# Optimization experiments

Measured on AMD Instinct MI355X. Metric: run time of the kernel, lower is better.

## Reference

```python
import jax, jax.numpy as jnp
import numpy as np

N_NODES = 100000
N_FEAT = 256
HIDDEN = 16
N_CLASSES = 16
N_EDGES = 3200000


def setup_inputs() -> dict:
    key = jax.random.key(0)
    k = jax.random.split(key, 7)
    x = jax.random.normal(k[0], (N_NODES, N_FEAT), dtype=jnp.float32)
    edge_index = jax.random.randint(k[1], (2, N_EDGES), 0, N_NODES, dtype=jnp.int32)
    # GCNConv: linear (no bias) + bias added after aggregation
    s1 = 1.0 / np.sqrt(N_FEAT)
    W1 = jax.random.uniform(k[2], (N_FEAT, HIDDEN), jnp.float32, -s1, s1)
    b1 = jnp.zeros((HIDDEN,), jnp.float32)
    # SAGEConv: lin_l (on aggregated neighbors, with bias) + lin_r (root)
    s2 = 1.0 / np.sqrt(HIDDEN)
    Wl = jax.random.uniform(k[3], (HIDDEN, N_CLASSES), jnp.float32, -s2, s2)
    Wr = jax.random.uniform(k[4], (HIDDEN, N_CLASSES), jnp.float32, -s2, s2)
    b2 = jax.random.uniform(k[5], (N_CLASSES,), jnp.float32, -s2, s2)
    return {"x": x, "edge_index": edge_index, "W1": W1, "b1": b1,
            "Wl": Wl, "Wr": Wr, "b2": b2}


def reference(x, edge_index, W1, b1, Wl, Wr, b2):
    N = x.shape[0]
    src, dst = edge_index[0], edge_index[1]

    # ---- GCNConv(num_features -> hidden): transform, add self-loops,
    # symmetric normalization, sum-aggregate, add bias ----
    h = x @ W1  # [N, H]
    loop = jnp.arange(N, dtype=src.dtype)
    src2 = jnp.concatenate([src, loop])
    dst2 = jnp.concatenate([dst, loop])
    ones = jnp.ones(src2.shape[0], dtype=h.dtype)
    deg = jax.ops.segment_sum(ones, dst2, num_segments=N)  # in-degree incl. self-loop
    dinv = jnp.where(deg > 0, jax.lax.rsqrt(deg), 0.0)
    norm = dinv[src2] * dinv[dst2]  # [E+N]
    msgs = h[src2] * norm[:, None]
    h1 = jax.ops.segment_sum(msgs, dst2, num_segments=N) + b1  # [N, H]

    # ---- SAGEConv(hidden -> num_classes, aggr='mean') ----
    cnt = jax.ops.segment_sum(jnp.ones(src.shape[0], dtype=h1.dtype), dst, num_segments=N)
    agg = jax.ops.segment_sum(h1[src], dst, num_segments=N)
    agg = agg / jnp.maximum(cnt, 1.0)[:, None]  # mean over neighbors
    out = agg @ Wl + h1 @ Wr + b2  # [N, C]

    return jax.nn.log_softmax(out, axis=1)
```

## Files before the change

### kernel.cpp

```cpp
#include <hip/hip_runtime.h>
#include <cstddef>

#define NF 256
#define NH 16
#define NC 16

#define BN    128
#define BSH   7
#define BMSK  127
#define CAP   4608
#define AVLEN 32
#define ACH   (256*AVLEN)
#define NBMAX 800

typedef __attribute__((ext_vector_type(8))) short bf16x8;
typedef __attribute__((ext_vector_type(4))) float f32x4;

__device__ inline short f2bf(float f) {
    union { float f; unsigned int u; } v; v.f = f;
    const unsigned int r = v.u + 0x7FFFu + ((v.u >> 16) & 1u);
    return (short)(r >> 16);
}
__device__ inline float bf2f(unsigned short u) {
    union { unsigned int i; float f; } v; v.i = ((unsigned int)u) << 16;
    return v.f;
}

__global__ __launch_bounds__(256) void bucketA_kernel(
    const int* __restrict__ src, const int* __restrict__ dst,
    unsigned int* __restrict__ bfill, unsigned int* __restrict__ bpairs,
    int E, int NBK)
{
    __shared__ unsigned int hist[NBMAX];
    __shared__ unsigned int sbase[NBMAX];
    __shared__ unsigned int gpos[NBMAX];
    __shared__ unsigned int tmp[1024];
    __shared__ unsigned int reorder[ACH];
    __shared__ unsigned short wbid[ACH];

    const int tid = threadIdx.x;
    for (int i = tid; i < NBMAX; i += 256) hist[i] = 0u;
    __syncthreads();

    const int base = blockIdx.x * ACH;
    unsigned int pv[AVLEN];
    unsigned int ps[AVLEN];
    #pragma unroll
    for (int l = 0; l < AVLEN; ++l) {
        const int e = base + l * 256 + tid;
        if (e < E) {
            const unsigned int s = (unsigned int)src[e];
            const unsigned int d = (unsigned int)dst[e];
            const unsigned int b = d >> BSH;
            pv[l] = (s << BSH) | (d & BMSK);
            const unsigned int slot = atomicAdd(&hist[b], 1u);
            ps[l] = (slot << 10) | b;
        } else {
            ps[l] = 0xFFFFFFFFu;
        }
    }
    __syncthreads();

    for (int i = tid; i < 1024; i += 256) tmp[i] = (i < NBK) ? hist[i] : 0u;
    __syncthreads();
    for (int off = 1; off < 1024; off <<= 1) {
        unsigned int v0 = 0, v1 = 0, v2 = 0, v3 = 0;
        const int i0 = tid, i1 = tid + 256, i2 = tid + 512, i3 = tid + 768;
        if (i0 >= off) v0 = tmp[i0 - off];
        if (i1 >= off) v1 = tmp[i1 - off];
        if (i2 >= off) v2 = tmp[i2 - off];
        if (i3 >= off) v3 = tmp[i3 - off];
        __syncthreads();
        tmp[i0] += v0; tmp[i1] += v1; tmp[i2] += v2; tmp[i3] += v3;
        __syncthreads();
    }
    for (int i = tid; i < NBK; i += 256) {
        const unsigned int h = hist[i];
        sbase[i] = tmp[i] - h;
        if (h) gpos[i] = atomicAdd(&bfill[i], h);
    }
    const int cc = (base + ACH <= E) ? ACH : (E - base);
    __syncthreads();

    #pragma unroll
    for (int l = 0; l < AVLEN; ++l) {
        if (ps[l] != 0xFFFFFFFFu) {
            const unsigned int b = ps[l] & 1023u;
            const unsigned int i = sbase[b] + (ps[l] >> 10);
            reorder[i] = pv[l];
            wbid[i] = (unsigned short)b;
        }
    }
    __syncthreads();

    for (int i = tid; i < cc; i += 256) {
        const unsigned int b = wbid[i];
        const unsigned int g = gpos[b] + ((unsigned int)i - sbase[b]);
        if (g < CAP) bpairs[(size_t)b * CAP + g] = reorder[i];
    }
}

__global__ __launch_bounds__(256) void bucketB_kernel(
    const unsigned int* __restrict__ bfill, unsigned int* __restrict__ bpairs,
    int* __restrict__ rowptr, int* __restrict__ cnt, float* __restrict__ dinv,
    int N)
{
    __shared__ unsigned int pairs[CAP];
    __shared__ unsigned int ssorted[CAP];
    __shared__ unsigned int hist[BN];
    __shared__ unsigned int scan[BN];
    __shared__ unsigned int cursor[BN];

    const int tid = threadIdx.x;
    const int b = blockIdx.x;
    const size_t bbase = (size_t)b * CAP;
    unsigned int m = bfill[b]; if (m > CAP) m = CAP;

    if (tid < BN) hist[tid] = 0u;
    __syncthreads();

    for (unsigned int i = tid; i < m; i += 256) {
        const unsigned int p = bpairs[bbase + i];
        pairs[i] = p;
        atomicAdd(&hist[p & BMSK], 1u);
    }
    __syncthreads();

    if (tid < BN) scan[tid] = hist[tid];
    __syncthreads();
    for (int off = 1; off < BN; off <<= 1) {
        unsigned int v = 0;
        if (tid < BN && tid >= off) v = scan[tid - off];
        __syncthreads();
        if (tid < BN) scan[tid] += v;
        __syncthreads();
    }
    if (tid < BN) cursor[tid] = scan[tid] - hist[tid];
    __syncthreads();

    for (unsigned int i = tid; i < m; i += 256) {
        const unsigned int p = pairs[i];
        const unsigned int pos = atomicAdd(&cursor[p & BMSK], 1u);
        ssorted[pos] = p >> BSH;
    }
    __syncthreads();

    for (unsigned int i = tid; i < m; i += 256)
        bpairs[bbase + i] = ssorted[i];

    if (tid < BN) {
        const int n = b * BN + tid;
        if (n < N) {
            const unsigned int h = hist[tid];
            cnt[n] = (int)h;
            dinv[n] = rsqrtf((float)h + 1.0f);
            rowptr[n] = (int)(b * CAP + (scan[tid] - h));
        }
    }
}

__global__ __launch_bounds__(256) void gemm1_mfma_kernel(
    const float* __restrict__ x, const float* __restrict__ W1,
    const float* __restrict__ dinv, unsigned short* __restrict__ hs_bf, int N)
{
    const int lane = threadIdx.x & 63;
    const int wave = threadIdx.x >> 6;
    const int quad = lane >> 4;
    const int mn   = lane & 15;

    bf16x8 bfrag[8];
    #pragma unroll
    for (int kc = 0; kc < 8; ++kc) {
        #pragma unroll
        for (int j = 0; j < 8; ++j) {
            const int k = kc * 32 + quad * 8 + j;
            bfrag[kc][j] = f2bf(W1[k * NH + mn]);
        }
    }

    const int tile = blockIdx.x * 4 + wave;
    if (tile * 16 >= N) return;
    const int n0 = tile * 16;

    f32x4 acc = {0.f, 0.f, 0.f, 0.f};
    const float* xrow = x + (size_t)(n0 + mn) * NF + quad * 8;
    #pragma unroll
    for (int kc = 0; kc < 8; ++kc) {
        const float4 lo = *(const float4*)(xrow + kc * 32);
        const float4 hi = *(const float4*)(xrow + kc * 32 + 4);
        bf16x8 af;
        af[0] = f2bf(lo.x); af[1] = f2bf(lo.y); af[2] = f2bf(lo.z); af[3] = f2bf(lo.w);
        af[4] = f2bf(hi.x); af[5] = f2bf(hi.y); af[6] = f2bf(hi.z); af[7] = f2bf(hi.w);
        acc = __builtin_amdgcn_mfma_f32_16x16x32_bf16(af, bfrag[kc], acc, 0, 0, 0);
    }

    const float4 dv = *(const float4*)(dinv + n0 + quad * 4);
    const float d[4] = {dv.x, dv.y, dv.z, dv.w};
    #pragma unroll
    for (int r = 0; r < 4; ++r) {
        const int row = quad * 4 + r;
        hs_bf[(size_t)(n0 + row) * NH + mn] = (unsigned short)f2bf(acc[r] * d[r]);
    }
}

__global__ __launch_bounds__(256) void gcn_gather_kernel(
    const unsigned short* __restrict__ hs_bf, const unsigned int* __restrict__ csrc,
    const int* __restrict__ rowptr, const int* __restrict__ cnt,
    const float* __restrict__ dinv, const float* __restrict__ b1,
    unsigned short* __restrict__ h1_bf, int N)
{
    const int tid = threadIdx.x;
    const int n = blockIdx.x * 16 + (tid >> 4);
    if (n >= N) return;
    const int j = tid & 15;
    const int start = rowptr[n];
    const int end = start + cnt[n];

    float acc = bf2f(hs_bf[(size_t)n * NH + j]);
    int k = start;
    for (; k + 16 <= end; k += 16) {
        const int myi = (int)csrc[k + j];
        float s = 0.f;
        #pragma unroll
        for (int u = 0; u < 16; ++u) {
            const int sidx = __shfl(myi, u, 16);
            s += bf2f(hs_bf[(size_t)sidx * NH + j]);
        }
        acc += s;
    }
    for (; k < end; ++k)
        acc += bf2f(hs_bf[(size_t)csrc[k] * NH + j]);

    h1_bf[(size_t)n * NH + j] = (unsigned short)f2bf(b1[j] + dinv[n] * acc);
}

__global__ __launch_bounds__(256) void sage_out_kernel(
    const unsigned short* __restrict__ h1_bf, const unsigned int* __restrict__ csrc,
    const int* __restrict__ rowptr, const int* __restrict__ cnt,
    const float* __restrict__ Wl, const float* __restrict__ Wr,
    const float* __restrict__ b2, float* __restrict__ out, int N)
{
    __shared__ float wls[NH * NC];
    __shared__ float wrs[NH * NC];
    __shared__ float b2s[NC];
    const int tid = threadIdx.x;
    if (tid < NH * NC) { wls[tid] = Wl[tid]; wrs[tid] = Wr[tid]; }
    if (tid < NC) b2s[tid] = b2[tid];
    __syncthreads();

    const int n = blockIdx.x * 16 + (tid >> 4);
    if (n >= N) return;
    const int j = tid & 15;
    const int start = rowptr[n];
    const int deg = cnt[n];
    const int end = start + deg;

    float acc = 0.f;
    int k = start;
    for (; k + 16 <= end; k += 16) {
        const int myi = (int)csrc[k + j];
        float s = 0.f;
        #pragma unroll
        for (int u = 0; u < 16; ++u) {
            const int sidx = __shfl(myi, u, 16);
            s += bf2f(h1_bf[(size_t)sidx * NH + j]);
        }
        acc += s;
    }
    for (; k < end; ++k)
        acc += bf2f(h1_bf[(size_t)csrc[k] * NH + j]);

    const float aggj = acc / fmaxf((float)deg, 1.0f);
    const float h1j  = bf2f(h1_bf[(size_t)n * NH + j]);

    float o = b2s[j];
    #pragma unroll
    for (int kk = 0; kk < NH; ++kk) {
        const float a  = __shfl(aggj, kk, 16);
        const float hh = __shfl(h1j,  kk, 16);
        o += a * wls[kk * NC + j] + hh * wrs[kk * NC + j];
    }

    float m = o;
    #pragma unroll
    for (int off = 1; off < 16; off <<= 1) m = fmaxf(m, __shfl_xor(m, off, 16));
    const float ex = expf(o - m);
    float ssum = ex;
    #pragma unroll
    for (int off = 1; off < 16; off <<= 1) ssum += __shfl_xor(ssum, off, 16);

    out[(size_t)n * NC + j] = (o - m) - logf(ssum);
}

extern "C" void kernel_launch(void* const* d_in, const int* in_sizes, int n_in,
                              void* d_out, int out_size, void* d_ws, size_t ws_size,
                              hipStream_t stream)
{
    const float* x  = (const float*)d_in[0];
    const int*   ei = (const int*)d_in[1];
    const float* W1 = (const float*)d_in[2];
    const float* b1 = (const float*)d_in[3];
    const float* Wl = (const float*)d_in[4];
    const float* Wr = (const float*)d_in[5];
    const float* b2 = (const float*)d_in[6];
    float* out = (float*)d_out;

    const int N = in_sizes[0] / NF;
    const int E = in_sizes[1] / 2;
    const int* src = ei;
    const int* dst = ei + E;

    const int NBK = (N + BN - 1) / BN;

    unsigned short* hs_bf = (unsigned short*)d_ws;
    unsigned short* h1_bf = hs_bf + (size_t)N * NH;
    float* dinv   = (float*)(h1_bf + (size_t)N * NH);
    int*   cnt    = (int*)(dinv + N);
    int*   rowptr = cnt + N;
    unsigned int* bfill  = (unsigned int*)(rowptr + N);
    unsigned int* bpairs = bfill + 1024;

    hipMemsetAsync(bfill, 0, (size_t)NBK * sizeof(unsigned int), stream);

    bucketA_kernel<<<(E + ACH - 1) / ACH, 256, 0, stream>>>(src, dst, bfill, bpairs, E, NBK);
    bucketB_kernel<<<NBK, 256, 0, stream>>>(bfill, bpairs, rowptr, cnt, dinv, N);

    const int tiles = (N + 15) / 16;
    gemm1_mfma_kernel<<<(tiles + 3) / 4, 256, 0, stream>>>(x, W1, dinv, hs_bf, N);

    const int nodeBlk = (N + 15) / 16;
    gcn_gather_kernel<<<nodeBlk, 256, 0, stream>>>(hs_bf, bpairs, rowptr, cnt, dinv, b1, h1_bf, N);
    sage_out_kernel<<<nodeBlk, 256, 0, stream>>>(h1_bf, bpairs, rowptr, cnt, Wl, Wr, b2, out, N);
}
```

Measured before the change: 319.2 us.

## Sub-sort edges by source range, use nontemporal accesses, shrink bucketing chunk

Bucket sort now orders each destination's edges into 8 sub-bins by the high bits of the source index, aiming to improve gather locality in the aggregation kernels. Streaming loads and stores of edge lists, x, and output use nontemporal hints to reduce cache pollution. The first bucketing pass halves its per-block chunk, which raises block count and lowers register pressure. The trade-off is a larger 1024-entry scan in the second pass and more partial-bucket writes.

```diff
diff --git a/kernel.cpp b/kernel.cpp
--- a/kernel.cpp
+++ b/kernel.cpp
@@ -9,9 +9,11 @@
 #define BSH   7
 #define BMSK  127
 #define CAP   4608
-#define AVLEN 32
+#define AVLEN 16
 #define ACH   (256*AVLEN)
 #define NBMAX 800
+#define NW    8
+#define SWSH  14
 
 typedef __attribute__((ext_vector_type(8))) short bf16x8;
 typedef __attribute__((ext_vector_type(4))) float f32x4;
@@ -49,8 +51,8 @@
     for (int l = 0; l < AVLEN; ++l) {
         const int e = base + l * 256 + tid;
         if (e < E) {
-            const unsigned int s = (unsigned int)src[e];
-            const unsigned int d = (unsigned int)dst[e];
+            const unsigned int s = (unsigned int)__builtin_nontemporal_load(&src[e]);
+            const unsigned int d = (unsigned int)__builtin_nontemporal_load(&dst[e]);
             const unsigned int b = d >> BSH;
             pv[l] = (s << BSH) | (d & BMSK);
             const unsigned int slot = atomicAdd(&hist[b], 1u);
@@ -107,54 +109,62 @@
 {
     __shared__ unsigned int pairs[CAP];
     __shared__ unsigned int ssorted[CAP];
-    __shared__ unsigned int hist[BN];
-    __shared__ unsigned int scan[BN];
-    __shared__ unsigned int cursor[BN];
+    __shared__ unsigned int hist[BN * NW];
+    __shared__ unsigned int scan[BN * NW];
+    __shared__ unsigned int cursor[BN * NW];
 
     const int tid = threadIdx.x;
     const int b = blockIdx.x;
     const size_t bbase = (size_t)b * CAP;
     unsigned int m = bfill[b]; if (m > CAP) m = CAP;
 
-    if (tid < BN) hist[tid] = 0u;
+    for (int i = tid; i < BN * NW; i += 256) hist[i] = 0u;
     __syncthreads();
 
     for (unsigned int i = tid; i < m; i += 256) {
-        const unsigned int p = bpairs[bbase + i];
+        const unsigned int p = __builtin_nontemporal_load(&bpairs[bbase + i]);
         pairs[i] = p;
-        atomicAdd(&hist[p & BMSK], 1u);
-    }
-    __syncthreads();
-
-    if (tid < BN) scan[tid] = hist[tid];
-    __syncthreads();
-    for (int off = 1; off < BN; off <<= 1) {
-        unsigned int v = 0;
-        if (tid < BN && tid >= off) v = scan[tid - off];
+        const unsigned int key = ((p & BMSK) << 3) | ((p >> BSH) >> SWSH);
+        atomicAdd(&hist[key], 1u);
+    }
+    __syncthreads();
+
+    for (int i = tid; i < 1024; i += 256) scan[i] = hist[i];
+    __syncthreads();
+    for (int off = 1; off < 1024; off <<= 1) {
+        unsigned int v0 = 0, v1 = 0, v2 = 0, v3 = 0;
+        const int i0 = tid, i1 = tid + 256, i2 = tid + 512, i3 = tid + 768;
+        if (i0 >= off) v0 = scan[i0 - off];
+        if (i1 >= off) v1 = scan[i1 - off];
+        if (i2 >= off) v2 = scan[i2 - off];
+        if (i3 >= off) v3 = scan[i3 - off];
         __syncthreads();
-        if (tid < BN) scan[tid] += v;
+        scan[i0] += v0; scan[i1] += v1; scan[i2] += v2; scan[i3] += v3;
         __syncthreads();
     }
-    if (tid < BN) cursor[tid] = scan[tid] - hist[tid];
+    for (int i = tid; i < 1024; i += 256) cursor[i] = scan[i] - hist[i];
     __syncthreads();
 
     for (unsigned int i = tid; i < m; i += 256) {
         const unsigned int p = pairs[i];
-        const unsigned int pos = atomicAdd(&cursor[p & BMSK], 1u);
+        const unsigned int key = ((p & BMSK) << 3) | ((p >> BSH) >> SWSH);
+        const unsigned int pos = atomicAdd(&cursor[key], 1u);
         ssorted[pos] = p >> BSH;
     }
     __syncthreads();
 
     for (unsigned int i = tid; i < m; i += 256)
-        bpairs[bbase + i] = ssorted[i];
+        __builtin_nontemporal_store(ssorted[i], &bpairs[bbase + i]);
 
     if (tid < BN) {
         const int n = b * BN + tid;
         if (n < N) {
-            const unsigned int h = hist[tid];
+            unsigned int h = 0;
+            #pragma unroll
+            for (int w = 0; w < NW; ++w) h += hist[tid * NW + w];
             cnt[n] = (int)h;
             dinv[n] = rsqrtf((float)h + 1.0f);
-            rowptr[n] = (int)(b * CAP + (scan[tid] - h));
+            rowptr[n] = (int)(b * CAP + (scan[tid * NW] - hist[tid * NW]));
         }
     }
 }
@@ -186,20 +196,19 @@
     const float* xrow = x + (size_t)(n0 + mn) * NF + quad * 8;
     #pragma unroll
     for (int kc = 0; kc < 8; ++kc) {
-        const float4 lo = *(const float4*)(xrow + kc * 32);
-        const float4 hi = *(const float4*)(xrow + kc * 32 + 4);
+        const f32x4 lo = __builtin_nontemporal_load((const f32x4*)(xrow + kc * 32));
+        const f32x4 hi = __builtin_nontemporal_load((const f32x4*)(xrow + kc * 32 + 4));
         bf16x8 af;
-        af[0] = f2bf(lo.x); af[1] = f2bf(lo.y); af[2] = f2bf(lo.z); af[3] = f2bf(lo.w);
-        af[4] = f2bf(hi.x); af[5] = f2bf(hi.y); af[6] = f2bf(hi.z); af[7] = f2bf(hi.w);
+        af[0] = f2bf(lo[0]); af[1] = f2bf(lo[1]); af[2] = f2bf(lo[2]); af[3] = f2bf(lo[3]);
+        af[4] = f2bf(hi[0]); af[5] = f2bf(hi[1]); af[6] = f2bf(hi[2]); af[7] = f2bf(hi[3]);
         acc = __builtin_amdgcn_mfma_f32_16x16x32_bf16(af, bfrag[kc], acc, 0, 0, 0);
     }
 
-    const float4 dv = *(const float4*)(dinv + n0 + quad * 4);
-    const float d[4] = {dv.x, dv.y, dv.z, dv.w};
+    const f32x4 dv = *(const f32x4*)(dinv + n0 + quad * 4);
     #pragma unroll
     for (int r = 0; r < 4; ++r) {
         const int row = quad * 4 + r;
-        hs_bf[(size_t)(n0 + row) * NH + mn] = (unsigned short)f2bf(acc[r] * d[r]);
+        hs_bf[(size_t)(n0 + row) * NH + mn] = (unsigned short)f2bf(acc[r] * dv[r]);
     }
 }
 
@@ -219,7 +228,7 @@
     float acc = bf2f(hs_bf[(size_t)n * NH + j]);
     int k = start;
     for (; k + 16 <= end; k += 16) {
-        const int myi = (int)csrc[k + j];
+        const int myi = (int)__builtin_nontemporal_load(&csrc[k + j]);
         float s = 0.f;
         #pragma unroll
         for (int u = 0; u < 16; ++u) {
@@ -258,7 +267,7 @@
     float acc = 0.f;
     int k = start;
     for (; k + 16 <= end; k += 16) {
-        const int myi = (int)csrc[k + j];
+        const int myi = (int)__builtin_nontemporal_load(&csrc[k + j]);
         float s = 0.f;
         #pragma unroll
         for (int u = 0; u < 16; ++u) {
@@ -289,7 +298,7 @@
     #pragma unroll
     for (int off = 1; off < 16; off <<= 1) ssum += __shfl_xor(ssum, off, 16);
 
-    out[(size_t)n * NC + j] = (o - m) - logf(ssum);
+    __builtin_nontemporal_store((o - m) - logf(ssum), &out[(size_t)n * NC + j]);
 }
 
 extern "C" void kernel_launch(void* const* d_in, const int* in_sizes, int n_in,
```

Result: slower. 342.6 us (+7.3%).
